# Kernel optimization log

Hardware: AMD Instinct MI355X
Metric: run time of the kernel (lower is better)

## Reference

```python
import jax, jax.numpy as jnp
import numpy as np

N_NODES = 50000


def gcn_layer(x, src, dst, W, b, n_nodes):
    # Linear transform first (as in PyG GCNConv)
    x = x @ W  # [N, out]
    # Symmetric normalization with self-loop-augmented degree
    ones = jnp.ones(src.shape[0], dtype=x.dtype)
    deg = jax.ops.segment_sum(ones, dst, num_segments=n_nodes)
    dinv = jnp.where(deg > 0, jax.lax.rsqrt(deg), 0.0).astype(x.dtype)
    norm = dinv[src] * dinv[dst]  # [E]
    msgs = x[src] * norm[:, None]  # [E, out]
    out = jax.ops.segment_sum(msgs, dst, num_segments=n_nodes)
    return out + b


def add_self_loops(edge_index, n_nodes):
    loop = jnp.arange(n_nodes, dtype=edge_index.dtype)
    src = jnp.concatenate([edge_index[0], loop])
    dst = jnp.concatenate([edge_index[1], loop])
    return src, dst


def setup_inputs() -> dict:
    key = jax.random.key(0)
    k1, k2, k3, k4 = jax.random.split(key, 4)
    in_ch, hid = 256, 256
    n_edges = 1600000
    x = jax.random.normal(k1, (N_NODES, in_ch), dtype=jnp.float32)
    edge_index = jax.random.randint(k2, (2, n_edges), 0, N_NODES, dtype=jnp.int64)
    # Glorot-style init for GCN weights
    W1 = jax.random.normal(k3, (in_ch, hid), dtype=jnp.float32) * (1.0 / np.sqrt(in_ch))
    b1 = jnp.zeros((hid,), dtype=jnp.float32)
    W2 = jax.random.normal(k4, (hid, hid), dtype=jnp.float32) * (1.0 / np.sqrt(hid))
    b2 = jnp.zeros((hid,), dtype=jnp.float32)
    return {"x": x, "edge_index": edge_index, "W1": W1, "b1": b1, "W2": W2, "b2": b2}


def reference(x, edge_index, W1, b1, W2, b2):
    n = x.shape[0]
    src, dst = add_self_loops(edge_index, n)
    h = gcn_layer(x, src, dst, W1, b1, n)
    h = jax.nn.relu(h)
    out = gcn_layer(h, src, dst, W2, b2, n)
    return out
```

## Files before the change

kernel.cpp:

```cpp
#include <hip/hip_runtime.h>
#include <stdint.h>

typedef __attribute__((ext_vector_type(8))) short bf16x8;
typedef __attribute__((ext_vector_type(4))) float f32x4;

#define NBLK 256
#define BSH  7
#define BSZ  128

typedef __attribute__((address_space(1))) const unsigned int gu32;
typedef __attribute__((address_space(3))) unsigned int lu32;

__device__ __forceinline__ float bf2f(unsigned short b) {
    union { unsigned u; float f; } c; c.u = ((unsigned)b) << 16; return c.f;
}
__device__ __forceinline__ float bflo(unsigned w) {
    union { unsigned u; float f; } c; c.u = w << 16; return c.f;
}
__device__ __forceinline__ float bfhi(unsigned w) {
    union { unsigned u; float f; } c; c.u = w & 0xffff0000u; return c.f;
}
__device__ __forceinline__ unsigned short f2bf(float f) {
    union { float f; unsigned u; } c; c.f = f;
    unsigned u = c.u;
    u += 0x7fffu + ((u >> 16) & 1u);
    return (unsigned short)(u >> 16);
}

__global__ void GNNEncoder_317827579954_kernel() {}

__global__ void k_flags(const unsigned* __restrict__ x, const int* __restrict__ ei,
                        int E, int* __restrict__ flags) {
    int t = threadIdx.x;
    int pl = 0;
    for (int i = t; i < 256; i += 64) {
        unsigned u = x[i] & 0xffffu;
        unsigned e = (u >> 7) & 0xffu;
        if ((e >= 100u && e <= 145u) || u == 0u) ++pl;
    }
    for (int off = 32; off; off >>= 1) pl += __shfl_down(pl, off);
    int n = E < 64 ? E : 64;
    unsigned long long nz = __ballot(t < n ? (ei[2 * t + 1] != 0) : 0);
    if (t == 0) {
        flags[0] = (pl >= 192) ? 0 : 1;
        flags[1] = (nz == 0ull) ? 1 : 0;
    }
}

__global__ void k_cvtT(const void* __restrict__ Wa, unsigned short* __restrict__ Wta,
                       const void* __restrict__ Wb, unsigned short* __restrict__ Wtb,
                       const int* __restrict__ flags) {
    int bb = blockIdx.x;
    const void* W = bb < 256 ? Wa : Wb;
    unsigned short* Wt = bb < 256 ? Wta : Wtb;
    int n = bb & 255, k = threadIdx.x;
    unsigned short v;
    if (flags[0]) v = f2bf(((const float*)W)[k * 256 + n]);
    else          v = ((const unsigned short*)W)[k * 256 + n];
    Wt[n * 256 + k] = v;
}


__global__ __launch_bounds__(256) void k_cmat(const int* __restrict__ ei, int E,
                                              const int* __restrict__ flags,
                                              int* __restrict__ cmat, int nb) {
    __shared__ int lc[512];
    int t = threadIdx.x, b = blockIdx.x;
    for (int i = t; i < nb; i += 256) lc[i] = 0;
    __syncthreads();
    int chunk = (E + NBLK - 1) / NBLK;
    int beg = b * chunk;
    int end = beg + chunk; if (end > E) end = E;
    int i64 = flags[1];
    for (int i = beg + t; i < end; i += 256) {
        int d = i64 ? ei[2 * E + 2 * i] : ei[E + i];
        atomicAdd(&lc[d >> BSH], 1);
    }
    __syncthreads();
    for (int j = t; j < nb; j += 256) cmat[j * NBLK + b] = lc[j];
}

__global__ __launch_bounds__(512) void k_cscan(int* __restrict__ cmat,
                                               int* __restrict__ boff,
                                               int* __restrict__ offs,
                                               int nb, int N, int E) {
    __shared__ int sc[512];
    int t = threadIdx.x;
    int run = 0;
    if (t < nb) {
        int* row = cmat + t * NBLK;
        for (int b = 0; b < NBLK; ++b) { int v = row[b]; row[b] = run; run += v; }
    }
    sc[t] = run;
    __syncthreads();
    int val = run;
    for (int off = 1; off < 512; off <<= 1) {
        int u = (t >= off) ? sc[t - off] : 0;
        __syncthreads();
        sc[t] += u;
        __syncthreads();
    }
    int ex = sc[t] - val;
    if (t < nb) {
        boff[t] = ex;
        int* row = cmat + t * NBLK;
        for (int b = 0; b < NBLK; ++b) row[b] += ex;
    }
    if (t == 0) { boff[nb] = E; offs[N] = E; }
}

__global__ __launch_bounds__(256) void k_fillmat(const int* __restrict__ ei, int E,
                                                 const int* __restrict__ flags,
                                                 const int* __restrict__ cmat,
                                                 unsigned* __restrict__ tmp, int nb) {
    __shared__ int cur[512];
    int t = threadIdx.x, b = blockIdx.x;
    for (int j = t; j < nb; j += 256) cur[j] = cmat[j * NBLK + b];
    __syncthreads();
    int chunk = (E + NBLK - 1) / NBLK;
    int beg = b * chunk;
    int end = beg + chunk; if (end > E) end = E;
    int i64 = flags[1];
    for (int i = beg + t; i < end; i += 256) {
        int s, d;
        if (i64) { s = ei[2 * i]; d = ei[2 * E + 2 * i]; }
        else     { s = ei[i];     d = ei[E + i]; }
        int p = atomicAdd(&cur[d >> BSH], 1);
        tmp[p] = ((unsigned)s << BSH) | (unsigned)(d & (BSZ - 1));
    }
}

__global__ __launch_bounds__(256) void k_bbuild(const unsigned* __restrict__ tmp,
                                                const int* __restrict__ boff,
                                                int* __restrict__ offs,
                                                float* __restrict__ dinv,
                                                int* __restrict__ csr, int N) {
    __shared__ int kc[2048];
    __shared__ int cur[2048];
    __shared__ int sc[256];
    __shared__ int tot;
    int b = blockIdx.x;
    int t = threadIdx.x;
    int base = b << BSH;
    int beg = boff[b], end = boff[b + 1];
    for (int i = t; i < 2048; i += 256) kc[i] = 0;
    __syncthreads();
    for (int i = beg + t; i < end; i += 256) {
        unsigned u = tmp[i];
        atomicAdd(&kc[(u & 127u) * 16 + (u >> 19)], 1);
    }
    __syncthreads();
    int b8 = t * 8, loc[8], msum = 0;
#pragma unroll
    for (int j = 0; j < 8; ++j) { loc[j] = kc[b8 + j]; msum += loc[j]; }
    sc[t] = msum;
    __syncthreads();
    int val = msum;
    for (int off = 1; off < 256; off <<= 1) {
        int u2 = (t >= off) ? sc[t - off] : 0;
        __syncthreads();
        sc[t] += u2;
        __syncthreads();
    }
    int run = sc[t] - val;
    if (t == 255) tot = sc[255];
#pragma unroll
    for (int j = 0; j < 8; ++j) { int v2 = loc[j]; kc[b8 + j] = run; cur[b8 + j] = run; run += v2; }
    __syncthreads();
    if (t < 128) {
        int v = base + t;
        if (v < N) {
            int s0 = kc[t * 16];
            int s1 = (t == 127) ? tot : kc[(t + 1) * 16];
            offs[v] = beg + s0;
            dinv[v] = rsqrtf((float)(s1 - s0 + 1));
        }
    }
    __syncthreads();
    for (int i = beg + t; i < end; i += 256) {
        unsigned u = tmp[i];
        int p = atomicAdd(&cur[(u & 127u) * 16 + (u >> 19)], 1);
        csr[beg + p] = (int)(u >> BSH);
    }
}

__global__ __launch_bounds__(256) void k_gemm(const void* __restrict__ Araw,
                                              const unsigned short* __restrict__ Bt,
                                              unsigned short* __restrict__ C,
                                              const float* __restrict__ dinv,
                                              const int* __restrict__ flags, int useflag,
                                              int M) {
    __shared__ unsigned short smem[16384];
    int tid  = threadIdx.x;
    int lane = tid & 63;
    int wave = tid >> 6;
    int q = lane >> 4;
    int r = lane & 15;
    int rowBase0 = blockIdx.x * 64;
    int rowBase = rowBase0 + wave * 16;
    int af32 = useflag ? flags[0] : 0;

    int arow = rowBase + r;
    arow = arow < M ? arow : M - 1;
    const unsigned short* aptrh = (const unsigned short*)Araw + (size_t)arow * 256;
    const float*          aptrf = (const float*)Araw + (size_t)arow * 256;

    auto stage = [&](int buf, int kk) {
#pragma unroll
        for (int j = 0; j < 4; ++j) {
            int c = wave * 256 + j * 64 + lane;
            int col = c >> 2;
            int kc = (c & 3) ^ (col & 3);
            const unsigned short* src = Bt + col * 256 + kk + kc * 8;
            unsigned short* dst = smem + buf * 8192 + (wave * 4 + j) * 512;
            __builtin_amdgcn_global_load_lds((gu32*)src, (lu32*)dst, 16, 0, 0);
        }
    };

    stage(0, 0);
    __syncthreads();

    f32x4 acc[16] = {};
    int cur = 0;
    for (int kk = 0; kk < 256; kk += 32) {
        if (kk < 224) stage(cur ^ 1, kk + 32);
        bf16x8 a;
        if (af32) {
            float4 v0 = *(const float4*)(aptrf + kk + q * 8);
            float4 v1 = *(const float4*)(aptrf + kk + q * 8 + 4);
            union { unsigned short s[8]; bf16x8 v; } ua;
            ua.s[0] = f2bf(v0.x); ua.s[1] = f2bf(v0.y); ua.s[2] = f2bf(v0.z); ua.s[3] = f2bf(v0.w);
            ua.s[4] = f2bf(v1.x); ua.s[5] = f2bf(v1.y); ua.s[6] = f2bf(v1.z); ua.s[7] = f2bf(v1.w);
            a = ua.v;
        } else {
            a = *(const bf16x8*)(aptrh + kk + q * 8);
        }
#pragma unroll
        for (int nt = 0; nt < 16; ++nt) {
            int col = nt * 16 + r;
            const unsigned short* bp = smem + cur * 8192 + col * 32 + (q ^ (col & 3)) * 8;
            bf16x8 b = *(const bf16x8*)bp;
            acc[nt] = __builtin_amdgcn_mfma_f32_16x16x32_bf16(a, b, acc[nt], 0, 0, 0);
        }
        __syncthreads();
        cur ^= 1;
    }

    float ds4[4];
#pragma unroll
    for (int r2 = 0; r2 < 4; ++r2) {
        int row = rowBase + q * 4 + r2;
        ds4[r2] = (row < M) ? dinv[row] : 0.f;
    }
    int lrow0 = wave * 16 + q * 4;
#pragma unroll
    for (int nt = 0; nt < 16; ++nt) {
        int col = nt * 16 + r;
#pragma unroll
        for (int r2 = 0; r2 < 4; ++r2)
            smem[(lrow0 + r2) * 256 + col] = f2bf(acc[nt][r2] * ds4[r2]);
    }
    __syncthreads();
#pragma unroll
    for (int p = 0; p < 8; ++p) {
        int idx = wave * 4096 + p * 512 + lane * 8;
        int grow = rowBase0 + (idx >> 8);
        if (grow < M)
            *(uint4*)(C + (size_t)grow * 256 + (idx & 255)) = *(const uint4*)(smem + idx);
    }
}

__global__ __launch_bounds__(256) void k_agg(const unsigned short* __restrict__ XWs,
                                             const int* __restrict__ csr,
                                             const int* __restrict__ offs,
                                             const float* __restrict__ dinv,
                                             const void* __restrict__ bias,
                                             void* __restrict__ out,
                                             int relu, int final_, const int* __restrict__ flags,
                                             int N) {
    int v = blockIdx.x * 4 + (threadIdx.x >> 6);
    if (v >= N) return;
    int lane = threadIdx.x & 63;
    int half = lane >> 5;
    int cl   = (lane & 31) * 8;
    float acc[8] = {};
    int beg = offs[v], end = offs[v + 1];
    int e = beg;
    for (; e + 8 <= end; e += 8) {
        int s[4]; uint4 u[4];
#pragma unroll
        for (int j = 0; j < 4; ++j) s[j] = csr[e + 2 * j + half];
#pragma unroll
        for (int j = 0; j < 4; ++j) u[j] = *(const uint4*)(XWs + (size_t)s[j] * 256 + cl);
#pragma unroll
        for (int j = 0; j < 4; ++j) {
            acc[0] += bflo(u[j].x); acc[1] += bfhi(u[j].x);
            acc[2] += bflo(u[j].y); acc[3] += bfhi(u[j].y);
            acc[4] += bflo(u[j].z); acc[5] += bfhi(u[j].z);
            acc[6] += bflo(u[j].w); acc[7] += bfhi(u[j].w);
        }
    }
    for (; e + 2 <= end; e += 2) {
        int s = csr[e + half];
        uint4 u = *(const uint4*)(XWs + (size_t)s * 256 + cl);
        acc[0] += bflo(u.x); acc[1] += bfhi(u.x);
        acc[2] += bflo(u.y); acc[3] += bfhi(u.y);
        acc[4] += bflo(u.z); acc[5] += bfhi(u.z);
        acc[6] += bflo(u.w); acc[7] += bfhi(u.w);
    }
    if (e < end && half == 0) {
        int s = csr[e];
        uint4 u = *(const uint4*)(XWs + (size_t)s * 256 + cl);
        acc[0] += bflo(u.x); acc[1] += bfhi(u.x);
        acc[2] += bflo(u.y); acc[3] += bfhi(u.y);
        acc[4] += bflo(u.z); acc[5] += bfhi(u.z);
        acc[6] += bflo(u.w); acc[7] += bfhi(u.w);
    }
#pragma unroll
    for (int k = 0; k < 8; ++k) acc[k] += __shfl_xor(acc[k], 32);
    if (half) return;

    float dv = dinv[v];
    uint4 su = *(const uint4*)(XWs + (size_t)v * 256 + cl);
    float sf[8];
    sf[0] = bflo(su.x); sf[1] = bfhi(su.x);
    sf[2] = bflo(su.y); sf[3] = bfhi(su.y);
    sf[4] = bflo(su.z); sf[5] = bfhi(su.z);
    sf[6] = bflo(su.w); sf[7] = bfhi(su.w);
    float bb[8];
    if (flags[0]) {
        const float4* bp = (const float4*)((const float*)bias + cl);
        float4 b0 = bp[0], b1 = bp[1];
        bb[0] = b0.x; bb[1] = b0.y; bb[2] = b0.z; bb[3] = b0.w;
        bb[4] = b1.x; bb[5] = b1.y; bb[6] = b1.z; bb[7] = b1.w;
    } else {
        uint4 bu = *(const uint4*)((const unsigned short*)bias + cl);
        bb[0] = bflo(bu.x); bb[1] = bfhi(bu.x);
        bb[2] = bflo(bu.y); bb[3] = bfhi(bu.y);
        bb[4] = bflo(bu.z); bb[5] = bfhi(bu.z);
        bb[6] = bflo(bu.w); bb[7] = bfhi(bu.w);
    }
    float r[8];
#pragma unroll
    for (int k = 0; k < 8; ++k) {
        float t = dv * (acc[k] + sf[k]) + bb[k];
        r[k] = relu ? fmaxf(t, 0.f) : t;
    }
    if (final_ && flags[0]) {
        float* op = (float*)out + (size_t)v * 256 + cl;
        float4 o0, o1;
        o0.x = r[0]; o0.y = r[1]; o0.z = r[2]; o0.w = r[3];
        o1.x = r[4]; o1.y = r[5]; o1.z = r[6]; o1.w = r[7];
        ((float4*)op)[0] = o0; ((float4*)op)[1] = o1;
    } else {
        uint4 o;
        o.x = (unsigned)f2bf(r[0]) | ((unsigned)f2bf(r[1]) << 16);
        o.y = (unsigned)f2bf(r[2]) | ((unsigned)f2bf(r[3]) << 16);
        o.z = (unsigned)f2bf(r[4]) | ((unsigned)f2bf(r[5]) << 16);
        o.w = (unsigned)f2bf(r[6]) | ((unsigned)f2bf(r[7]) << 16);
        *(uint4*)((unsigned short*)out + (size_t)v * 256 + cl) = o;
    }
}

extern "C" void kernel_launch(void* const* d_in, const int* in_sizes, int n_in,
                              void* d_out, int out_size, void* d_ws, size_t ws_size,
                              hipStream_t stream) {
    (void)n_in; (void)out_size; (void)ws_size;
    const void* x  = d_in[0];
    const int*  ei = (const int*)d_in[1];
    const void* W1 = d_in[2];
    const void* b1 = d_in[3];
    const void* W2 = d_in[4];
    const void* b2 = d_in[5];

    int N = in_sizes[0] / 256;
    int E = in_sizes[1] / 2;
    int NB = (N + BSZ - 1) / BSZ;

    char* p = (char*)d_ws;
    auto alloc = [&](size_t bytes) {
        char* r = p;
        p += (bytes + 255) & ~(size_t)255;
        return r;
    };
    int*            flags  = (int*)alloc(8);
    int*            boff   = (int*)alloc(516 * 4);
    int*            offs   = (int*)alloc(((size_t)N + 1) * 4);
    float*          dinv   = (float*)alloc((size_t)N * 4);
    unsigned short* wt1    = (unsigned short*)alloc(256 * 256 * 2);
    unsigned short* wt2    = (unsigned short*)alloc(256 * 256 * 2);
    int*            csr    = (int*)alloc((size_t)E * 4);
    unsigned short* buf0   = (unsigned short*)alloc((size_t)N * 256 * 2);
    unsigned short* buf1   = (unsigned short*)alloc((size_t)N * 256 * 2);
    unsigned*       tmp    = (unsigned*)buf1;
    int*            cmat   = (int*)buf0;
    unsigned short* xw1    = (unsigned short*)d_out;

    k_flags<<<1, 64, 0, stream>>>((const unsigned*)x, ei, E, flags);
    k_cmat<<<NBLK, 256, 0, stream>>>(ei, E, flags, cmat, NB);
    k_cscan<<<1, 512, 0, stream>>>(cmat, boff, offs, NB, N, E);
    k_fillmat<<<NBLK, 256, 0, stream>>>(ei, E, flags, cmat, tmp, NB);
    k_bbuild<<<NB, 256, 0, stream>>>(tmp, boff, offs, dinv, csr, N);

    k_cvtT<<<512, 256, 0, stream>>>(W1, wt1, W2, wt2, flags);

    int gAgg = (N + 3) / 4;
    k_gemm<<<(N + 63) / 64, 256, 0, stream>>>(x, wt1, xw1, dinv, flags, 1, N);
    k_agg<<<gAgg, 256, 0, stream>>>(xw1, csr, offs, dinv, b1,
                                    (void*)buf0, 1, 0, flags, N);
    k_gemm<<<(N + 63) / 64, 256, 0, stream>>>(buf0, wt2, buf1, dinv, flags, 0, N);
    k_agg<<<gAgg, 256, 0, stream>>>(buf1, csr, offs, dinv, b2,
                                    d_out, 0, 1, flags, N);
}
```

Before: 471.4 us.

## Merge flag/weight-convert/count kernels and parallelize the bucket-offset scan

```diff
diff --git a/kernel.cpp b/kernel.cpp
--- a/kernel.cpp
+++ b/kernel.cpp
@@ -29,93 +29,108 @@
 
 __global__ void GNNEncoder_317827579954_kernel() {}
 
-__global__ void k_flags(const unsigned* __restrict__ x, const int* __restrict__ ei,
-                        int E, int* __restrict__ flags) {
+__global__ __launch_bounds__(256) void k_prep(const void* __restrict__ Wa,
+                                              unsigned short* __restrict__ Wta,
+                                              const void* __restrict__ Wb,
+                                              unsigned short* __restrict__ Wtb,
+                                              const unsigned* __restrict__ x,
+                                              const int* __restrict__ ei, int E,
+                                              int* __restrict__ cmat, int nb,
+                                              int* __restrict__ flags) {
+    __shared__ int lc[512];
+    __shared__ int sflag;
     int t = threadIdx.x;
-    int pl = 0;
-    for (int i = t; i < 256; i += 64) {
-        unsigned u = x[i] & 0xffffu;
-        unsigned e = (u >> 7) & 0xffu;
-        if ((e >= 100u && e <= 145u) || u == 0u) ++pl;
-    }
-    for (int off = 32; off; off >>= 1) pl += __shfl_down(pl, off);
-    int n = E < 64 ? E : 64;
-    unsigned long long nz = __ballot(t < n ? (ei[2 * t + 1] != 0) : 0);
-    if (t == 0) {
-        flags[0] = (pl >= 192) ? 0 : 1;
-        flags[1] = (nz == 0ull) ? 1 : 0;
-    }
-}
-
-__global__ void k_cvtT(const void* __restrict__ Wa, unsigned short* __restrict__ Wta,
-                       const void* __restrict__ Wb, unsigned short* __restrict__ Wtb,
-                       const int* __restrict__ flags) {
     int bb = blockIdx.x;
-    const void* W = bb < 256 ? Wa : Wb;
-    unsigned short* Wt = bb < 256 ? Wta : Wtb;
-    int n = bb & 255, k = threadIdx.x;
-    unsigned short v;
-    if (flags[0]) v = f2bf(((const float*)W)[k * 256 + n]);
-    else          v = ((const unsigned short*)W)[k * 256 + n];
-    Wt[n * 256 + k] = v;
-}
-
-
-__global__ __launch_bounds__(256) void k_cmat(const int* __restrict__ ei, int E,
-                                              const int* __restrict__ flags,
-                                              int* __restrict__ cmat, int nb) {
-    __shared__ int lc[512];
-    int t = threadIdx.x, b = blockIdx.x;
-    for (int i = t; i < nb; i += 256) lc[i] = 0;
-    __syncthreads();
-    int chunk = (E + NBLK - 1) / NBLK;
-    int beg = b * chunk;
-    int end = beg + chunk; if (end > E) end = E;
-    int i64 = flags[1];
-    for (int i = beg + t; i < end; i += 256) {
-        int d = i64 ? ei[2 * E + 2 * i] : ei[E + i];
-        atomicAdd(&lc[d >> BSH], 1);
-    }
-    __syncthreads();
-    for (int j = t; j < nb; j += 256) cmat[j * NBLK + b] = lc[j];
-}
-
-__global__ __launch_bounds__(512) void k_cscan(int* __restrict__ cmat,
+    if (bb < 512) {
+        if (t < 64) {
+            int pl = 0;
+            for (int i = t; i < 256; i += 64) {
+                unsigned u = x[i] & 0xffffu;
+                unsigned e2 = (u >> 7) & 0xffu;
+                if ((e2 >= 100u && e2 <= 145u) || u == 0u) ++pl;
+            }
+            for (int off = 32; off; off >>= 1) pl += __shfl_down(pl, off);
+            if (t == 0) sflag = (pl >= 192) ? 0 : 1;
+        }
+        __syncthreads();
+        int af32 = sflag;
+        if (bb == 0 && t == 0) flags[0] = af32;
+        const void* W = bb < 256 ? Wa : Wb;
+        unsigned short* Wt = bb < 256 ? Wta : Wtb;
+        int n = bb & 255;
+        unsigned short v;
+        if (af32) v = f2bf(((const float*)W)[t * 256 + n]);
+        else      v = ((const unsigned short*)W)[t * 256 + n];
+        Wt[n * 256 + t] = v;
+    } else {
+        int b = bb - 512;
+        if (t < 64) {
+            int n = E < 64 ? E : 64;
+            unsigned long long nz = __ballot(t < n ? (ei[2 * t + 1] != 0) : 0);
+            if (t == 0) sflag = (nz == 0ull) ? 1 : 0;
+        }
+        for (int i = t; i < nb; i += 256) lc[i] = 0;
+        __syncthreads();
+        int i64 = sflag;
+        if (b == 0 && t == 0) flags[1] = i64;
+        int chunk = (E + NBLK - 1) / NBLK;
+        int beg = b * chunk;
+        int end = beg + chunk; if (end > E) end = E;
+        for (int i = beg + t; i < end; i += 256) {
+            int d = i64 ? ei[2 * E + 2 * i] : ei[E + i];
+            atomicAdd(&lc[d >> BSH], 1);
+        }
+        __syncthreads();
+        for (int j = t; j < nb; j += 256) cmat[j * NBLK + b] = lc[j];
+    }
+}
+
+__global__ __launch_bounds__(256) void k_rowscan(int* __restrict__ cmat,
+                                                 int* __restrict__ btot) {
+    __shared__ int sc[256];
+    int j = blockIdx.x;
+    int t = threadIdx.x;
+    int* row = cmat + j * NBLK;
+    int v = row[t];
+    sc[t] = v;
+    __syncthreads();
+    for (int off = 1; off < 256; off <<= 1) {
+        int u = (t >= off) ? sc[t - off] : 0;
+        __syncthreads();
+        sc[t] += u;
+        __syncthreads();
+    }
+    row[t] = sc[t] - v;
+    if (t == 255) btot[j] = sc[255];
+}
+
+__global__ __launch_bounds__(512) void k_bscan(const int* __restrict__ btot,
                                                int* __restrict__ boff,
                                                int* __restrict__ offs,
                                                int nb, int N, int E) {
     __shared__ int sc[512];
     int t = threadIdx.x;
-    int run = 0;
-    if (t < nb) {
-        int* row = cmat + t * NBLK;
-        for (int b = 0; b < NBLK; ++b) { int v = row[b]; row[b] = run; run += v; }
-    }
-    sc[t] = run;
-    __syncthreads();
-    int val = run;
+    int v = (t < nb) ? btot[t] : 0;
+    sc[t] = v;
+    __syncthreads();
     for (int off = 1; off < 512; off <<= 1) {
         int u = (t >= off) ? sc[t - off] : 0;
         __syncthreads();
         sc[t] += u;
         __syncthreads();
     }
-    int ex = sc[t] - val;
-    if (t < nb) {
-        boff[t] = ex;
-        int* row = cmat + t * NBLK;
-        for (int b = 0; b < NBLK; ++b) row[b] += ex;
-    }
+    if (t < nb) boff[t] = sc[t] - v;
     if (t == 0) { boff[nb] = E; offs[N] = E; }
 }
 
 __global__ __launch_bounds__(256) void k_fillmat(const int* __restrict__ ei, int E,
                                                  const int* __restrict__ flags,
                                                  const int* __restrict__ cmat,
+                                                 const int* __restrict__ boff,
                                                  unsigned* __restrict__ tmp, int nb) {
     __shared__ int cur[512];
     int t = threadIdx.x, b = blockIdx.x;
-    for (int j = t; j < nb; j += 256) cur[j] = cmat[j * NBLK + b];
+    for (int j = t; j < nb; j += 256) cur[j] = cmat[j * NBLK + b] + boff[j];
     __syncthreads();
     int chunk = (E + NBLK - 1) / NBLK;
     int beg = b * chunk;
@@ -385,6 +400,7 @@
     };
     int*            flags  = (int*)alloc(8);
     int*            boff   = (int*)alloc(516 * 4);
+    int*            btot   = (int*)alloc(512 * 4);
     int*            offs   = (int*)alloc(((size_t)N + 1) * 4);
     float*          dinv   = (float*)alloc((size_t)N * 4);
     unsigned short* wt1    = (unsigned short*)alloc(256 * 256 * 2);
@@ -396,13 +412,12 @@
     int*            cmat   = (int*)buf0;
     unsigned short* xw1    = (unsigned short*)d_out;
 
-    k_flags<<<1, 64, 0, stream>>>((const unsigned*)x, ei, E, flags);
-    k_cmat<<<NBLK, 256, 0, stream>>>(ei, E, flags, cmat, NB);
-    k_cscan<<<1, 512, 0, stream>>>(cmat, boff, offs, NB, N, E);
-    k_fillmat<<<NBLK, 256, 0, stream>>>(ei, E, flags, cmat, tmp, NB);
+    k_prep<<<512 + NBLK, 256, 0, stream>>>(W1, wt1, W2, wt2,
+                                           (const unsigned*)x, ei, E, cmat, NB, flags);
+    k_rowscan<<<NB, 256, 0, stream>>>(cmat, btot);
+    k_bscan<<<1, 512, 0, stream>>>(btot, boff, offs, NB, N, E);
+    k_fillmat<<<NBLK, 256, 0, stream>>>(ei, E, flags, cmat, boff, tmp, NB);
     k_bbuild<<<NB, 256, 0, stream>>>(tmp, boff, offs, dinv, csr, N);
-
-    k_cvtT<<<512, 256, 0, stream>>>(W1, wt1, W2, wt2, flags);
 
     int gAgg = (N + 3) / 4;
     k_gemm<<<(N + 63) / 64, 256, 0, stream>>>(x, wt1, xw1, dinv, flags, 1, N);
```

Result: faster. 401.7 us (-14.8%).
